# Kernel tuning notes

Measured on AMD Instinct MI355X. Metric: run time of the kernel, lower is better.

The kernel has to match this reference:

```python
import jax, jax.numpy as jnp
import numpy as np

D_MODEL = 1024
NUM_HEADS = 16
HEAD_DIM = D_MODEL // NUM_HEADS
B, T = 4, 2048


def setup_inputs() -> dict:
    key = jax.random.key(0)
    k_x, k_wqkv, k_bqkv, k_wo, k_bo = jax.random.split(key, 5)
    s = 1.0 / np.sqrt(D_MODEL)
    return {
        "x": jax.random.normal(k_x, (B, T, D_MODEL), jnp.float32),
        "w_qkv": jax.random.uniform(k_wqkv, (D_MODEL, 3 * D_MODEL), jnp.float32, -s, s),
        "b_qkv": jax.random.uniform(k_bqkv, (3 * D_MODEL,), jnp.float32, -s, s),
        "w_out": jax.random.uniform(k_wo, (D_MODEL, D_MODEL), jnp.float32, -s, s),
        "b_out": jax.random.uniform(k_bo, (D_MODEL,), jnp.float32, -s, s),
    }


def reference(x, w_qkv, b_qkv, w_out, b_out):
    Bb, Tt, C = x.shape
    qkv = x @ w_qkv + b_qkv  # (B, T, 3C)
    q, k, v = jnp.split(qkv, 3, axis=-1)
    # (B, H, T, hd)
    def heads(t):
        return t.reshape(Bb, Tt, NUM_HEADS, HEAD_DIM).transpose(0, 2, 1, 3)
    q, k, v = heads(q), heads(k), heads(v)
    scale = 1.0 / np.sqrt(HEAD_DIM).astype(np.float32)
    att = jnp.einsum("bhqd,bhkd->bhqk", q, k) * scale
    causal = jnp.tril(jnp.ones((Tt, Tt), dtype=bool))
    att = jnp.where(causal, att, -jnp.inf)
    att = jax.nn.softmax(att, axis=-1)
    y = jnp.einsum("bhqk,bhkd->bhqd", att, v)
    y = y.transpose(0, 2, 1, 3).reshape(Bb, Tt, C)
    return y @ w_out + b_out
```

## Files before the change

kernel.cpp:

```cpp
#include <hip/hip_runtime.h>
#include <hip/hip_bf16.h>
#include <math.h>

#define D_MODEL 1024
#define NHEADS  16
#define HDIM    64
#define BATCH   4
#define SEQ     2048

typedef __attribute__((ext_vector_type(8))) short bf16x8;
typedef __attribute__((ext_vector_type(4))) float f32x4;

#if __has_builtin(__builtin_amdgcn_exp2f)
#define EXP2(x) __builtin_amdgcn_exp2f(x)
#else
#define EXP2(x) exp2f(x)
#endif

__device__ __forceinline__ unsigned short f2bf(float f) {
  union { float f; unsigned u; } v; v.f = f;
  unsigned r = v.u + 0x7FFFu + ((v.u >> 16) & 1u);
  return (unsigned short)(r >> 16);
}

__device__ __forceinline__ unsigned cvtpk(float lo, float hi) {
  unsigned r;
  asm("v_cvt_pk_bf16_f32 %0, %1, %2" : "=v"(r) : "v"(lo), "v"(hi));
  return r;
}

__device__ __forceinline__ void load_lds16(const unsigned short* g, unsigned short* l) {
  __builtin_amdgcn_global_load_lds(
      (const __attribute__((address_space(1))) unsigned int*)g,
      (__attribute__((address_space(3))) unsigned int*)l, 16, 0, 0);
}

__global__ __launch_bounds__(256) void cast_kernel(
    const float* __restrict__ in, unsigned short* __restrict__ out)
{
  const int idx = (blockIdx.x * 256 + threadIdx.x) * 8;
  float4 a = *(const float4*)&in[idx];
  float4 b = *(const float4*)&in[idx + 4];
  alignas(16) unsigned short t[8] = {
    f2bf(a.x), f2bf(a.y), f2bf(a.z), f2bf(a.w),
    f2bf(b.x), f2bf(b.y), f2bf(b.z), f2bf(b.w)};
  *(uint4*)&out[idx] = *(uint4*)t;
}

__global__ __launch_bounds__(256) void transpose_cast(
    const float* __restrict__ W, unsigned short* __restrict__ WT, int N)
{
  __shared__ float t[64][65];
  const int k0 = blockIdx.y * 64, n0 = blockIdx.x * 64;
  const int tid = threadIdx.x;
  const int r = tid >> 2, c0 = (tid & 3) * 16;
  #pragma unroll
  for (int i = 0; i < 16; i += 4) {
    float4 f = *(const float4*)&W[(size_t)(k0 + r) * N + n0 + c0 + i];
    t[r][c0+i] = f.x; t[r][c0+i+1] = f.y; t[r][c0+i+2] = f.z; t[r][c0+i+3] = f.w;
  }
  __syncthreads();
  #pragma unroll
  for (int i = 0; i < 16; i += 4) {
    alignas(8) unsigned short s[4] = {
      f2bf(t[c0+i][r]), f2bf(t[c0+i+1][r]), f2bf(t[c0+i+2][r]), f2bf(t[c0+i+3][r])};
    *(uint2*)&WT[(size_t)(n0 + r) * 1024 + k0 + c0 + i] = *(uint2*)s;
  }
}

#define BARRIER __builtin_amdgcn_s_barrier()
#define FENCE   asm volatile("" ::: "memory")
#define LGKM0   do { asm volatile("s_waitcnt lgkmcnt(0)" ::: "memory"); \
                     __builtin_amdgcn_sched_barrier(0); } while (0)

template<int MODE>
__global__ __launch_bounds__(512, 2) void gemm8p(
    const unsigned short* __restrict__ A,
    const unsigned short* __restrict__ Bt,
    const float* __restrict__ bias,
    unsigned short* __restrict__ Qb, unsigned short* __restrict__ Kb,
    unsigned short* __restrict__ Vb, float* __restrict__ Out)
{
  constexpr int N  = (MODE == 0) ? 3 * D_MODEL : D_MODEL;
  constexpr int NT = D_MODEL / 64;
  const int bn = blockIdx.x * 256;
  const int bm = blockIdx.y * 128;
  const int tid  = threadIdx.x;
  const int lane = tid & 63;
  const int w    = tid >> 6;
  const int quad = lane >> 4;
  const int l16  = lane & 15;
  const int wr = w >> 2, wc = w & 3;

  __shared__ __align__(16) unsigned short lds[49152];

  const int srow = lane >> 3;
  const int scol = ((lane & 7) ^ srow) * 8;
  const unsigned short* __restrict__ Ag = A  + (size_t)(bm + w*8 + srow) * D_MODEL + scol;
  const unsigned short* __restrict__ Bg = Bt + (size_t)(bn + w*8 + srow) * D_MODEL + scol;
  const int xs = (l16 & 7) * 8;

  f32x4 acc[4][4] = {};

  auto stageA = [&](int buf, int t2) {
    unsigned short* d = &lds[buf*8192 + w*512];
    const unsigned short* g = Ag + t2*64;
    load_lds16(g,                      d);
    load_lds16(g + (size_t)64*D_MODEL, d + 4096);
  };
  auto stageB = [&](int buf, int t2) {
    unsigned short* d = &lds[16384 + buf*16384 + w*512];
    const unsigned short* g = Bg + t2*64;
    #pragma unroll
    for (int c = 0; c < 4; c++)
      load_lds16(g + (size_t)c*64*D_MODEL, d + c*4096);
  };
  auto rdA = [&](int buf, int mi, int kk) {
    return *(const bf16x8*)&lds[buf*8192 +
        (wr*64 + mi*16 + l16)*64 + (((kk*4 + quad)*8) ^ xs)];
  };
  auto rdB = [&](int buf, int ni, int kk) {
    return *(const bf16x8*)&lds[16384 + buf*16384 +
        (wc*64 + ni*16 + l16)*64 + (((kk*4 + quad)*8) ^ xs)];
  };

  stageB(0, 0); stageA(0, 0);
  stageB(1, 1); stageA(1, 1);
  asm volatile("s_waitcnt vmcnt(6)" ::: "memory");
  BARRIER;
  FENCE;

  #pragma unroll 2
  for (int t = 0; t < NT; ++t) {
    const int cur  = t & 1;
    const bool pre = (t + 2 < NT);
    bf16x8 a0[2][2], a1[2][2], b0[2][2], b1[2][2];

    #pragma unroll
    for (int kk = 0; kk < 2; kk++)
      #pragma unroll
      for (int i = 0; i < 2; i++) { a0[i][kk] = rdA(cur, i, kk); b0[i][kk] = rdB(cur, i, kk); }
    BARRIER; LGKM0;
    __builtin_amdgcn_s_setprio(1);
    #pragma unroll
    for (int kk = 0; kk < 2; kk++)
      #pragma unroll
      for (int mi = 0; mi < 2; mi++)
        #pragma unroll
        for (int ni = 0; ni < 2; ni++)
          acc[mi][ni] = __builtin_amdgcn_mfma_f32_16x16x32_bf16(a0[mi][kk], b0[ni][kk], acc[mi][ni], 0, 0, 0);
    __builtin_amdgcn_s_setprio(0);
    BARRIER;

    #pragma unroll
    for (int kk = 0; kk < 2; kk++)
      #pragma unroll
      for (int i = 0; i < 2; i++) b1[i][kk] = rdB(cur, 2 + i, kk);
    BARRIER; LGKM0;
    __builtin_amdgcn_s_setprio(1);
    #pragma unroll
    for (int kk = 0; kk < 2; kk++)
      #pragma unroll
      for (int mi = 0; mi < 2; mi++)
        #pragma unroll
        for (int ni = 0; ni < 2; ni++)
          acc[mi][2+ni] = __builtin_amdgcn_mfma_f32_16x16x32_bf16(a0[mi][kk], b1[ni][kk], acc[mi][2+ni], 0, 0, 0);
    __builtin_amdgcn_s_setprio(0);
    BARRIER;

    #pragma unroll
    for (int kk = 0; kk < 2; kk++)
      #pragma unroll
      for (int i = 0; i < 2; i++) a1[i][kk] = rdA(cur, 2 + i, kk);
    if (pre) stageB(cur, t + 2);
    BARRIER; LGKM0;
    __builtin_amdgcn_s_setprio(1);
    #pragma unroll
    for (int kk = 0; kk < 2; kk++)
      #pragma unroll
      for (int mi = 0; mi < 2; mi++)
        #pragma unroll
        for (int ni = 0; ni < 2; ni++)
          acc[2+mi][ni] = __builtin_amdgcn_mfma_f32_16x16x32_bf16(a1[mi][kk], b0[ni][kk], acc[2+mi][ni], 0, 0, 0);
    __builtin_amdgcn_s_setprio(0);
    BARRIER;

    if (pre) {
      stageA(cur, t + 2);
      asm volatile("s_waitcnt vmcnt(6)" ::: "memory");
    } else {
      asm volatile("s_waitcnt vmcnt(0)" ::: "memory");
    }
    BARRIER;
    FENCE;
    __builtin_amdgcn_s_setprio(1);
    #pragma unroll
    for (int kk = 0; kk < 2; kk++)
      #pragma unroll
      for (int mi = 0; mi < 2; mi++)
        #pragma unroll
        for (int ni = 0; ni < 2; ni++)
          acc[2+mi][2+ni] = __builtin_amdgcn_mfma_f32_16x16x32_bf16(a1[mi][kk], b1[ni][kk], acc[2+mi][2+ni], 0, 0, 0);
    __builtin_amdgcn_s_setprio(0);
    BARRIER;
  }

  const int b   = bm >> 11;
  const int tl0 = (bm & (SEQ - 1));
  #pragma unroll
  for (int ni = 0; ni < 4; ni++) {
    const int n = bn + wc*64 + ni*16 + l16;
    const float bv = bias[n];
    #pragma unroll
    for (int mi = 0; mi < 4; mi++) {
      const int t0 = tl0 + wr*64 + mi*16 + quad*4;
      if (MODE == 0) {
        const int which = n >> 10;
        const int c = n & 1023;
        const int h = c >> 6, hd = c & 63;
        const size_t bhb = ((size_t)(b*NHEADS + h)) * (SEQ*HDIM);
        if (which == 2) {
          alignas(8) unsigned short pk[4];
          #pragma unroll
          for (int r = 0; r < 4; r++) pk[r] = f2bf(acc[mi][ni][r] + bv);
          *(uint2*)&Vb[bhb + (size_t)hd*SEQ + t0] = *(uint2*)pk;
        } else if (which == 0) {
          #pragma unroll
          for (int r = 0; r < 4; r++)
            Qb[bhb + (size_t)(t0 + r)*HDIM + hd] = f2bf((acc[mi][ni][r] + bv) * 0.18033688f);
        } else {
          #pragma unroll
          for (int r = 0; r < 4; r++)
            Kb[bhb + (size_t)(t0 + r)*HDIM + hd] = f2bf(acc[mi][ni][r] + bv);
        }
      } else {
        const int m = bm + wr*64 + mi*16 + quad*4;
        #pragma unroll
        for (int r = 0; r < 4; r++)
          Out[(size_t)(m + r) * N + n] = acc[mi][ni][r] + bv;
      }
    }
  }
}

__global__ __launch_bounds__(256) void attn_kernel(
    const unsigned short* __restrict__ Qb,
    const unsigned short* __restrict__ Kb,
    const unsigned short* __restrict__ Vt,
    unsigned short* __restrict__ Yb)
{
  const int bh   = blockIdx.x;
  const int Gp   = blockIdx.y;
  const int tid  = threadIdx.x;
  const int wave = tid >> 6;
  const int lane = tid & 63;
  const int quad = lane >> 4;
  const int l16  = lane & 15;

  __shared__ __align__(16) unsigned short Ks[2][64 * 64];
  __shared__ __align__(16) unsigned short Vs[2][64 * 64];
  __shared__ __align__(16) unsigned short Pl[8][16][72];

  const unsigned short* __restrict__ qb_ = Qb + (size_t)bh * (SEQ*HDIM);
  const unsigned short* __restrict__ kb_ = Kb + (size_t)bh * (SEQ*HDIM);
  const unsigned short* __restrict__ vb_ = Vt + (size_t)bh * (SEQ*HDIM);
  const int h = bh & (NHEADS - 1);
  const int b = bh >> 4;

  const short ob = (short)0x3F80;
  const bf16x8 ones = {ob,ob,ob,ob,ob,ob,ob,ob};

  const int srow = lane >> 3;
  const int scolswz = ((lane & 7) ^ srow) * 8;
  const int krow0 = wave * 16 + srow;
  const int xs = (l16 & 7) * 8;

  auto stage = [&](int buf, int it) {
    const int kb = it * 64;
    #pragma unroll
    for (int j = 0; j < 2; j++)
      load_lds16(kb_ + (size_t)(kb + krow0 + j*8)*HDIM + scolswz,
                 &Ks[buf][wave*1024 + j*512]);
    #pragma unroll
    for (int j = 0; j < 2; j++)
      load_lds16(vb_ + (size_t)(krow0 + j*8)*SEQ + kb + scolswz,
                 &Vs[buf][(wave*16 + j*8)*64]);
  };

  for (int half = 0; half < 2; half++) {
    const int qt = half ? (15 - Gp) : Gp;
    const int nt = 2 * qt + 2;
    const int qs0 = qt * 128 + wave * 32;
    const int myLast = 2 * qt + (wave >> 1);

    bf16x8 qf[2][2];
    #pragma unroll
    for (int t = 0; t < 2; t++)
      #pragma unroll
      for (int kk = 0; kk < 2; kk++)
        qf[t][kk] = *(const bf16x8*)(qb_ + (qs0 + t*16 + l16)*HDIM + kk*32 + quad*8);

    f32x4 acc[2][4] = {};
    float lrow[2][4] = {};

    stage(0, 0);
    __syncthreads();

    for (int it = 0; it < nt; it++) {
      const int cur = it & 1;

      if (it + 1 < nt) stage(cur ^ 1, it + 1);

      if (it <= myLast) {
        const int kb = it * 64;
        f32x4 sfr[4] = {}, sfr1[4] = {};
        __builtin_amdgcn_s_setprio(1);
        #pragma unroll
        for (int kk = 0; kk < 2; kk++)
          #pragma unroll
          for (int nf = 0; nf < 4; nf++) {
            const bf16x8 kf = *(const bf16x8*)&Ks[cur][(nf*16 + l16)*64 + ((kk*32 + quad*8) ^ xs)];
            sfr[nf]  = __builtin_amdgcn_mfma_f32_16x16x32_bf16(kf, qf[0][kk], sfr[nf], 0, 0, 0);
            sfr1[nf] = __builtin_amdgcn_mfma_f32_16x16x32_bf16(kf, qf[1][kk], sfr1[nf], 0, 0, 0);
          }
        __builtin_amdgcn_s_setprio(0);

        if (it == myLast) {
          #pragma unroll
          for (int nf = 0; nf < 4; nf++) {
            const int key = kb + nf*16 + quad*4;
            #pragma unroll
            for (int r = 0; r < 4; r++) {
              sfr[nf][r]  = (key + r > qs0 + l16)      ? -INFINITY : sfr[nf][r];
              sfr1[nf][r] = (key + r > qs0 + 16 + l16) ? -INFINITY : sfr1[nf][r];
            }
          }
        }

        #pragma unroll
        for (int nf = 0; nf < 4; nf++) {
          uint2 p0, p1;
          p0.x = cvtpk(EXP2(sfr[nf][0]),  EXP2(sfr[nf][1]));
          p0.y = cvtpk(EXP2(sfr[nf][2]),  EXP2(sfr[nf][3]));
          p1.x = cvtpk(EXP2(sfr1[nf][0]), EXP2(sfr1[nf][1]));
          p1.y = cvtpk(EXP2(sfr1[nf][2]), EXP2(sfr1[nf][3]));
          *(uint2*)&Pl[wave*2 + 0][l16][nf*16 + quad*4] = p0;
          *(uint2*)&Pl[wave*2 + 1][l16][nf*16 + quad*4] = p1;
        }

        #pragma unroll
        for (int t = 0; t < 2; t++) {
          f32x4 rsum = {};
          __builtin_amdgcn_s_setprio(1);
          #pragma unroll
          for (int kk = 0; kk < 2; kk++) {
            const bf16x8 pf = *(const bf16x8*)&Pl[wave*2 + t][l16][kk*32 + quad*8];
            #pragma unroll
            for (int nf = 0; nf < 4; nf++) {
              const bf16x8 vf = *(const bf16x8*)&Vs[cur][(nf*16 + l16)*64 + ((kk*32 + quad*8) ^ xs)];
              acc[t][nf] = __builtin_amdgcn_mfma_f32_16x16x32_bf16(pf, vf, acc[t][nf], 0, 0, 0);
            }
            rsum = __builtin_amdgcn_mfma_f32_16x16x32_bf16(pf, ones, rsum, 0, 0, 0);
          }
          __builtin_amdgcn_s_setprio(0);
          #pragma unroll
          for (int r = 0; r < 4; r++) lrow[t][r] += rsum[r];
        }
      }

      __syncthreads();
    }

    #pragma unroll
    for (int t = 0; t < 2; t++) {
      #pragma unroll
      for (int r = 0; r < 4; r++) {
        const float inv = 1.0f / lrow[t][r];
        const int trow = qs0 + t*16 + quad*4 + r;
        const size_t off = ((size_t)(b * SEQ + trow)) * D_MODEL + h * HDIM;
        #pragma unroll
        for (int nf = 0; nf < 4; nf++)
          Yb[off + nf*16 + l16] = f2bf(acc[t][nf][r] * inv);
      }
    }
  }
}

extern "C" void kernel_launch(void* const* d_in, const int* in_sizes, int n_in,
                              void* d_out, int out_size, void* d_ws, size_t ws_size,
                              hipStream_t stream) {
  const float* x     = (const float*)d_in[0];
  const float* w_qkv = (const float*)d_in[1];
  const float* b_qkv = (const float*)d_in[2];
  const float* w_out = (const float*)d_in[3];
  const float* b_out = (const float*)d_in[4];
  float* out = (float*)d_out;

  const size_t SZ = (size_t)BATCH * NHEADS * SEQ * HDIM;
  unsigned short* Qb  = (unsigned short*)d_ws;
  unsigned short* Kb  = Qb + SZ;
  unsigned short* Vb  = Kb + SZ;
  unsigned short* Xb  = Vb + SZ;
  unsigned short* Yb  = Xb;
  unsigned short* WqT = Xb + SZ;
  unsigned short* WoT = WqT + (size_t)3*D_MODEL*D_MODEL;

  cast_kernel<<<dim3((BATCH*SEQ*D_MODEL)/(256*8)), 256, 0, stream>>>(x, Xb);
  transpose_cast<<<dim3(3*D_MODEL/64, D_MODEL/64), 256, 0, stream>>>(w_qkv, WqT, 3*D_MODEL);
  transpose_cast<<<dim3(D_MODEL/64, D_MODEL/64), 256, 0, stream>>>(w_out, WoT, D_MODEL);

  gemm8p<0><<<dim3(3*D_MODEL/256, BATCH*SEQ/128), 512, 0, stream>>>(
      Xb, WqT, b_qkv, Qb, Kb, Vb, nullptr);
  attn_kernel<<<dim3(BATCH*NHEADS, 8), 256, 0, stream>>>(Qb, Kb, Vb, Yb);
  gemm8p<1><<<dim3(D_MODEL/256, BATCH*SEQ/128), 512, 0, stream>>>(
      Yb, WoT, b_out, nullptr, nullptr, nullptr, out);
}
```

Before: 252.2 us.

## Fuse prep kernels and simplify GEMM to double-buffered loop with XCD-aware block remap

Merges the input cast and both weight transpose-casts into one prep launch. The GEMM's hand-tuned four-phase pipeline (prefetch two tiles ahead, fine-grained barriers and waitcnts) is replaced by a plain double buffer: each iteration stages the next tile, runs 32 MFMAs, then waits at one __syncthreads. Block IDs are also remapped with an interleave of eight so neighbouring tiles land on the same XCD for better L2 reuse. The simpler loop drops the explicit load/compute interleaving and may expose more global-load latency, since the full-barrier sync waits on all outstanding loads.

```diff
diff --git a/kernel.cpp b/kernel.cpp
--- a/kernel.cpp
+++ b/kernel.cpp
@@ -35,24 +35,31 @@
       (__attribute__((address_space(3))) unsigned int*)l, 16, 0, 0);
 }
 
-__global__ __launch_bounds__(256) void cast_kernel(
-    const float* __restrict__ in, unsigned short* __restrict__ out)
-{
-  const int idx = (blockIdx.x * 256 + threadIdx.x) * 8;
-  float4 a = *(const float4*)&in[idx];
-  float4 b = *(const float4*)&in[idx + 4];
-  alignas(16) unsigned short t[8] = {
-    f2bf(a.x), f2bf(a.y), f2bf(a.z), f2bf(a.w),
-    f2bf(b.x), f2bf(b.y), f2bf(b.z), f2bf(b.w)};
-  *(uint4*)&out[idx] = *(uint4*)t;
-}
-
-__global__ __launch_bounds__(256) void transpose_cast(
-    const float* __restrict__ W, unsigned short* __restrict__ WT, int N)
+__global__ __launch_bounds__(256) void prep_kernel(
+    const float* __restrict__ x,     unsigned short* __restrict__ Xb,
+    const float* __restrict__ w_qkv, unsigned short* __restrict__ WqT,
+    const float* __restrict__ w_out, unsigned short* __restrict__ WoT)
 {
   __shared__ float t[64][65];
-  const int k0 = blockIdx.y * 64, n0 = blockIdx.x * 64;
+  const int id  = blockIdx.x;
   const int tid = threadIdx.x;
+
+  if (id < 4096) {
+    const int idx = (id * 256 + tid) * 8;
+    float4 a = *(const float4*)&x[idx];
+    float4 b = *(const float4*)&x[idx + 4];
+    alignas(16) unsigned short o[8] = {
+      f2bf(a.x), f2bf(a.y), f2bf(a.z), f2bf(a.w),
+      f2bf(b.x), f2bf(b.y), f2bf(b.z), f2bf(b.w)};
+    *(uint4*)&Xb[idx] = *(uint4*)o;
+    return;
+  }
+
+  const float* W; unsigned short* WT; int N, rblk;
+  if (id < 4096 + 768) { W = w_qkv; WT = WqT; N = 3 * D_MODEL; rblk = id - 4096; }
+  else                 { W = w_out; WT = WoT; N = D_MODEL;     rblk = id - 4864; }
+  const int gx = N / 64;
+  const int n0 = (rblk % gx) * 64, k0 = (rblk / gx) * 64;
   const int r = tid >> 2, c0 = (tid & 3) * 16;
   #pragma unroll
   for (int i = 0; i < 16; i += 4) {
@@ -68,23 +75,24 @@
   }
 }
 
-#define BARRIER __builtin_amdgcn_s_barrier()
-#define FENCE   asm volatile("" ::: "memory")
-#define LGKM0   do { asm volatile("s_waitcnt lgkmcnt(0)" ::: "memory"); \
-                     __builtin_amdgcn_sched_barrier(0); } while (0)
-
 template<int MODE>
-__global__ __launch_bounds__(512, 2) void gemm8p(
+__global__ __launch_bounds__(512, 2) void gemm_db(
     const unsigned short* __restrict__ A,
     const unsigned short* __restrict__ Bt,
     const float* __restrict__ bias,
     unsigned short* __restrict__ Qb, unsigned short* __restrict__ Kb,
     unsigned short* __restrict__ Vb, float* __restrict__ Out)
 {
-  constexpr int N  = (MODE == 0) ? 3 * D_MODEL : D_MODEL;
-  constexpr int NT = D_MODEL / 64;
-  const int bn = blockIdx.x * 256;
-  const int bm = blockIdx.y * 128;
+  constexpr int N   = (MODE == 0) ? 3 * D_MODEL : D_MODEL;
+  constexpr int NT  = D_MODEL / 64;
+  constexpr int GX  = N / 256;
+  constexpr int NWG = GX * (BATCH * SEQ / 128);
+
+  int id = blockIdx.y * GX + blockIdx.x;
+  id = (id & 7) * (NWG >> 3) + (id >> 3);
+  const int bn = (id % GX) * 256;
+  const int bm = (id / GX) * 128;
+
   const int tid  = threadIdx.x;
   const int lane = tid & 63;
   const int w    = tid >> 6;
@@ -102,18 +110,16 @@
 
   f32x4 acc[4][4] = {};
 
-  auto stageA = [&](int buf, int t2) {
-    unsigned short* d = &lds[buf*8192 + w*512];
-    const unsigned short* g = Ag + t2*64;
-    load_lds16(g,                      d);
-    load_lds16(g + (size_t)64*D_MODEL, d + 4096);
-  };
-  auto stageB = [&](int buf, int t2) {
-    unsigned short* d = &lds[16384 + buf*16384 + w*512];
-    const unsigned short* g = Bg + t2*64;
+  auto stageAll = [&](int buf, int t2) {
+    unsigned short* dA = &lds[buf*8192 + w*512];
+    unsigned short* dB = &lds[16384 + buf*16384 + w*512];
+    const unsigned short* gA = Ag + t2*64;
+    const unsigned short* gB = Bg + t2*64;
+    load_lds16(gA,                      dA);
+    load_lds16(gA + (size_t)64*D_MODEL, dA + 4096);
     #pragma unroll
     for (int c = 0; c < 4; c++)
-      load_lds16(g + (size_t)c*64*D_MODEL, d + c*4096);
+      load_lds16(gB + (size_t)c*64*D_MODEL, dB + c*4096);
   };
   auto rdA = [&](int buf, int mi, int kk) {
     return *(const bf16x8*)&lds[buf*8192 +
@@ -124,85 +130,30 @@
         (wc*64 + ni*16 + l16)*64 + (((kk*4 + quad)*8) ^ xs)];
   };
 
-  stageB(0, 0); stageA(0, 0);
-  stageB(1, 1); stageA(1, 1);
-  asm volatile("s_waitcnt vmcnt(6)" ::: "memory");
-  BARRIER;
-  FENCE;
-
-  #pragma unroll 2
+  stageAll(0, 0);
+  __syncthreads();
+
   for (int t = 0; t < NT; ++t) {
-    const int cur  = t & 1;
-    const bool pre = (t + 2 < NT);
-    bf16x8 a0[2][2], a1[2][2], b0[2][2], b1[2][2];
-
-    #pragma unroll
-    for (int kk = 0; kk < 2; kk++)
-      #pragma unroll
-      for (int i = 0; i < 2; i++) { a0[i][kk] = rdA(cur, i, kk); b0[i][kk] = rdB(cur, i, kk); }
-    BARRIER; LGKM0;
-    __builtin_amdgcn_s_setprio(1);
-    #pragma unroll
-    for (int kk = 0; kk < 2; kk++)
-      #pragma unroll
-      for (int mi = 0; mi < 2; mi++)
-        #pragma unroll
-        for (int ni = 0; ni < 2; ni++)
-          acc[mi][ni] = __builtin_amdgcn_mfma_f32_16x16x32_bf16(a0[mi][kk], b0[ni][kk], acc[mi][ni], 0, 0, 0);
-    __builtin_amdgcn_s_setprio(0);
-    BARRIER;
-
-    #pragma unroll
-    for (int kk = 0; kk < 2; kk++)
-      #pragma unroll
-      for (int i = 0; i < 2; i++) b1[i][kk] = rdB(cur, 2 + i, kk);
-    BARRIER; LGKM0;
-    __builtin_amdgcn_s_setprio(1);
-    #pragma unroll
-    for (int kk = 0; kk < 2; kk++)
-      #pragma unroll
-      for (int mi = 0; mi < 2; mi++)
-        #pragma unroll
-        for (int ni = 0; ni < 2; ni++)
-          acc[mi][2+ni] = __builtin_amdgcn_mfma_f32_16x16x32_bf16(a0[mi][kk], b1[ni][kk], acc[mi][2+ni], 0, 0, 0);
-    __builtin_amdgcn_s_setprio(0);
-    BARRIER;
-
-    #pragma unroll
-    for (int kk = 0; kk < 2; kk++)
-      #pragma unroll
-      for (int i = 0; i < 2; i++) a1[i][kk] = rdA(cur, 2 + i, kk);
-    if (pre) stageB(cur, t + 2);
-    BARRIER; LGKM0;
-    __builtin_amdgcn_s_setprio(1);
-    #pragma unroll
-    for (int kk = 0; kk < 2; kk++)
-      #pragma unroll
-      for (int mi = 0; mi < 2; mi++)
-        #pragma unroll
-        for (int ni = 0; ni < 2; ni++)
-          acc[2+mi][ni] = __builtin_amdgcn_mfma_f32_16x16x32_bf16(a1[mi][kk], b0[ni][kk], acc[2+mi][ni], 0, 0, 0);
-    __builtin_amdgcn_s_setprio(0);
-    BARRIER;
-
-    if (pre) {
-      stageA(cur, t + 2);
-      asm volatile("s_waitcnt vmcnt(6)" ::: "memory");
-    } else {
-      asm volatile("s_waitcnt vmcnt(0)" ::: "memory");
+    const int cur = t & 1;
+    if (t + 1 < NT) stageAll(cur ^ 1, t + 1);
+
+    #pragma unroll
+    for (int kk = 0; kk < 2; kk++) {
+      bf16x8 af[4], bfv[4];
+      #pragma unroll
+      for (int mi = 0; mi < 4; mi++) af[mi]  = rdA(cur, mi, kk);
+      #pragma unroll
+      for (int ni = 0; ni < 4; ni++) bfv[ni] = rdB(cur, ni, kk);
+      __builtin_amdgcn_s_setprio(1);
+      #pragma unroll
+      for (int mi = 0; mi < 4; mi++)
+        #pragma unroll
+        for (int ni = 0; ni < 4; ni++)
+          acc[mi][ni] = __builtin_amdgcn_mfma_f32_16x16x32_bf16(af[mi], bfv[ni], acc[mi][ni], 0, 0, 0);
+      __builtin_amdgcn_s_setprio(0);
     }
-    BARRIER;
-    FENCE;
-    __builtin_amdgcn_s_setprio(1);
-    #pragma unroll
-    for (int kk = 0; kk < 2; kk++)
-      #pragma unroll
-      for (int mi = 0; mi < 2; mi++)
-        #pragma unroll
-        for (int ni = 0; ni < 2; ni++)
-          acc[2+mi][2+ni] = __builtin_amdgcn_mfma_f32_16x16x32_bf16(a1[mi][kk], b1[ni][kk], acc[2+mi][2+ni], 0, 0, 0);
-    __builtin_amdgcn_s_setprio(0);
-    BARRIER;
+
+    __syncthreads();
   }
 
   const int b   = bm >> 11;
@@ -405,13 +356,12 @@
   unsigned short* WqT = Xb + SZ;
   unsigned short* WoT = WqT + (size_t)3*D_MODEL*D_MODEL;
 
-  cast_kernel<<<dim3((BATCH*SEQ*D_MODEL)/(256*8)), 256, 0, stream>>>(x, Xb);
-  transpose_cast<<<dim3(3*D_MODEL/64, D_MODEL/64), 256, 0, stream>>>(w_qkv, WqT, 3*D_MODEL);
-  transpose_cast<<<dim3(D_MODEL/64, D_MODEL/64), 256, 0, stream>>>(w_out, WoT, D_MODEL);
-
-  gemm8p<0><<<dim3(3*D_MODEL/256, BATCH*SEQ/128), 512, 0, stream>>>(
+  prep_kernel<<<dim3(4096 + 768 + 256), 256, 0, stream>>>(
+      x, Xb, w_qkv, WqT, w_out, WoT);
+
+  gemm_db<0><<<dim3(3*D_MODEL/256, BATCH*SEQ/128), 512, 0, stream>>>(
       Xb, WqT, b_qkv, Qb, Kb, Vb, nullptr);
   attn_kernel<<<dim3(BATCH*NHEADS, 8), 256, 0, stream>>>(Qb, Kb, Vb, Yb);
-  gemm8p<1><<<dim3(D_MODEL/256, BATCH*SEQ/128), 512, 0, stream>>>(
+  gemm_db<1><<<dim3(D_MODEL/256, BATCH*SEQ/128), 512, 0, stream>>>(
       Yb, WoT, b_out, nullptr, nullptr, nullptr, out);
 }
```

Result: faster. 245.4 us (-2.7%).
